# Kernel tuning notes

Measured on AMD Instinct MI355X. Metric: run time of the kernel, lower is better.

The kernel has to match this reference:

```python
import jax, jax.numpy as jnp
import numpy as np
from jax import lax

N = 50000
C = 8
HW = 11
E = 800000
BD = 4
LIN_DIM = C * (HW - 2) * (HW - 2) + BD  # 652
HID = 256
OUT = 5
EPS = 1e-5


def _layernorm(h, g, b):
    mu = jnp.mean(h, axis=-1, keepdims=True)
    var = jnp.var(h, axis=-1, keepdims=True)
    return (h - mu) * lax.rsqrt(var + EPS) * g + b


def setup_inputs() -> dict:
    key = jax.random.key(0)
    ks = jax.random.split(key, 20)
    x = jax.random.normal(ks[0], (N, C, HW, HW), dtype=jnp.float32)
    bd_pred = jax.random.normal(ks[1], (N, BD), dtype=jnp.float32)
    src = jax.random.randint(ks[2], (E,), 0, N)
    dst = jax.random.randint(ks[3], (E,), 0, N)
    dst = jnp.where(src == dst, (dst + 1) % N, dst)  # no self loops
    edge_index = jnp.stack([src, dst]).astype(jnp.int64)
    s = 0.02
    p = {
        'conv_self_w': jax.random.normal(ks[4], (C, C, 3, 3), jnp.float32) * s,
        'conv_self_b': jnp.zeros((C,), jnp.float32),
        'lin_w': jax.random.normal(ks[5], (HID, LIN_DIM), jnp.float32) * s,
        'lin_b': jnp.zeros((HID,), jnp.float32),
        'lin_self_w': jax.random.normal(ks[6], (HID, LIN_DIM), jnp.float32) * s,
        'lin_self_b': jnp.zeros((HID,), jnp.float32),
        'sage_l_w': jax.random.normal(ks[7], (3, HID, HID), jnp.float32) * s,
        'sage_l_b': jnp.zeros((3, HID), jnp.float32),
        'sage_r_w': jax.random.normal(ks[8], (3, HID, HID), jnp.float32) * s,
        'ln_g': jnp.ones((2, HID), jnp.float32),
        'ln_b': jnp.zeros((2, HID), jnp.float32),
        'mp1_w': jax.random.normal(ks[9], (HID, HID), jnp.float32) * s,
        'mp1_b': jnp.zeros((HID,), jnp.float32),
        'mp2_w': jax.random.normal(ks[10], (OUT, HID), jnp.float32) * s,
        'mp2_b': jnp.zeros((OUT,), jnp.float32),
    }
    return dict(x=x, bd_pred=bd_pred, edge_index=edge_index, **p)


def reference(x, bd_pred, edge_index, conv_self_w, conv_self_b, lin_w, lin_b,
              lin_self_w, lin_self_b, sage_l_w, sage_l_b, sage_r_w,
              ln_g, ln_b, mp1_w, mp1_b, mp2_w, mp2_b):
    n = x.shape[0]
    src, dst = edge_index[0], edge_index[1]

    # CustomConv layer 0: conv_self -> flatten -> hstack(bd_pred) -> relu -> two linears
    h = lax.conv_general_dilated(x, conv_self_w, (1, 1), 'VALID',
                                 dimension_numbers=('NCHW', 'OIHW', 'NCHW'))
    h = h + conv_self_b[None, :, None, None]
    h = jnp.concatenate([h.reshape(n, -1), bd_pred], axis=1)  # [N, 652]
    h = jax.nn.relu(h)
    self_x = h @ lin_self_w.T + lin_self_b
    neigh = h @ lin_w.T + lin_b
    h = self_x + jax.ops.segment_sum(neigh[src], dst, num_segments=n)  # aggr='add'

    # in-degree for SAGEConv mean aggregation
    deg = jax.ops.segment_sum(jnp.ones((src.shape[0],), h.dtype), dst, num_segments=n)
    deg = jnp.maximum(deg, 1.0)[:, None]

    emb = h
    for i in range(3):  # SAGEConv layers 1..3
        mean_agg = jax.ops.segment_sum(h[src], dst, num_segments=n) / deg
        h = mean_agg @ sage_l_w[i].T + sage_l_b[i] + h @ sage_r_w[i].T
        emb = h
        h = jax.nn.relu(h)
        # dropout p=0.25 is identity in eval mode
        if i != 2:
            h = _layernorm(h, ln_g[i], ln_b[i])

    z = h @ mp1_w.T + mp1_b
    z = z @ mp2_w.T + mp2_b
    return emb, jax.nn.log_softmax(z, axis=1)
```

## Files before the change

### kernel.cpp

```cpp
#include <hip/hip_runtime.h>
#include <hip/hip_bf16.h>
#include <stdint.h>

#define NN 50000
#define EE 800000

typedef unsigned short u16;
typedef __attribute__((ext_vector_type(4))) float f32x4;
typedef __attribute__((ext_vector_type(8))) short bf16x8;

__device__ __forceinline__ float bu2f(u16 u){ return __uint_as_float(((unsigned)u)<<16); }
__device__ __forceinline__ u16 f2bu(float f){
  unsigned u = __float_as_uint(f);
  u += 0x7fffu + ((u>>16)&1u);
  return (u16)(u>>16);
}
__device__ __forceinline__ float lo16f(unsigned u){ return __uint_as_float(u << 16); }
__device__ __forceinline__ float hi16f(unsigned u){ return __uint_as_float(u & 0xffff0000u); }

__global__ void sniff_kernel(const int* __restrict__ e, const u16* __restrict__ xu,
                             int* __restrict__ flags){
  __shared__ int nz, cnt;
  int t = threadIdx.x;
  if (t == 0){ nz = 0; cnt = 0; }
  __syncthreads();
  if (e[2*t + 1] != 0) atomicOr(&nz, 1);
  u16 u = xu[2*t];
  int ef = (u >> 7) & 0xFF;
  int ok = (u == 0) || (ef >= 118 && ef <= 132);
  atomicAdd(&cnt, ok);
  __syncthreads();
  if (t == 0){ flags[0] = (nz == 0) ? 1 : 0; flags[1] = (cnt >= 200) ? 1 : 0; }
}

__global__ void convert_edges_kernel(const void* __restrict__ ep, int* __restrict__ outp,
                                     const int* __restrict__ flags, int total){
  int i = blockIdx.x*256 + threadIdx.x;
  if (i >= total) return;
  if (flags[0]) outp[i] = (int)((const long long*)ep)[i];
  else          outp[i] = ((const int*)ep)[i];
}

struct CanonTab {
  const void* src[15];
  void*       dst[15];
  int rows[15];
  int sk[15];
  int dk[15];
  int tobf[15];
};

__global__ __launch_bounds__(256) void canon_params_kernel(CanonTab tab, const int* __restrict__ flags){
  int a = blockIdx.y;
  int isbf = flags[1];
  int rows = tab.rows[a], sk = tab.sk[a], dk = tab.dk[a], tobf = tab.tobf[a];
  int n = rows * dk;
  int base = (blockIdx.x*256 + threadIdx.x) * 8;
  if (base >= n) return;
  #pragma unroll
  for (int uu = 0; uu < 8; uu++){
    int i = base + uu;
    if (i >= n) break;
    int r = i / dk, c = i - r*dk;
    float v = 0.f;
    if (c < sk){
      size_t si = (size_t)r*sk + c;
      v = isbf ? bu2f(((const u16*)tab.src[a])[si]) : ((const float*)tab.src[a])[si];
    }
    if (tobf) ((u16*)tab.dst[a])[i] = f2bu(v);
    else      ((float*)tab.dst[a])[i] = v;
  }
}

__global__ __launch_bounds__(256) void conv_relu_kernel(
    const void* __restrict__ xraw, const void* __restrict__ bdraw,
    const float* __restrict__ cw, const float* __restrict__ cb,
    const int* __restrict__ flags, u16* __restrict__ h0){
  __shared__ float xs[968];
  __shared__ float wsm[576];
  __shared__ float bs[8];
  int n = blockIdx.x, t = threadIdx.x;
  int isbf = flags[1];
  if (isbf){
    const ushort4* xp = (const ushort4*)((const u16*)xraw + (size_t)n*968);
    if (t < 242){ ushort4 u = xp[t]; xs[4*t]=bu2f(u.x); xs[4*t+1]=bu2f(u.y); xs[4*t+2]=bu2f(u.z); xs[4*t+3]=bu2f(u.w); }
  } else {
    const float4* xp = (const float4*)((const float*)xraw + (size_t)n*968);
    if (t < 242){ float4 u = xp[t]; xs[4*t]=u.x; xs[4*t+1]=u.y; xs[4*t+2]=u.z; xs[4*t+3]=u.w; }
  }
  if (t < 144){ float4 u = ((const float4*)cw)[t]; wsm[4*t]=u.x; wsm[4*t+1]=u.y; wsm[4*t+2]=u.z; wsm[4*t+3]=u.w; }
  if (t < 8) bs[t] = cb[t];
  __syncthreads();
  u16* outr = h0 + (size_t)n*704;
  if (t < 216){
    int co = t & 7;
    int rowid = t >> 3;
    int oi = rowid / 3;
    int og = rowid - oi*3;
    float wreg[72];
    #pragma unroll
    for (int q = 0; q < 72; q++) wreg[q] = wsm[co*72 + q];
    float a0 = bs[co], a1 = a0, a2 = a0;
    #pragma unroll
    for (int ci = 0; ci < 8; ci++){
      #pragma unroll
      for (int ki = 0; ki < 3; ki++){
        const float* xb = xs + ci*121 + (oi+ki)*11 + og*3;
        float x0=xb[0], x1=xb[1], x2=xb[2], x3=xb[3], x4=xb[4];
        float w0=wreg[ci*9+ki*3+0], w1=wreg[ci*9+ki*3+1], w2=wreg[ci*9+ki*3+2];
        a0 += x0*w0 + x1*w1 + x2*w2;
        a1 += x1*w0 + x2*w1 + x3*w2;
        a2 += x2*w0 + x3*w1 + x4*w2;
      }
    }
    int colbase = co*81 + oi*9 + og*3;
    outr[colbase+0] = f2bu(fmaxf(a0, 0.f));
    outr[colbase+1] = f2bu(fmaxf(a1, 0.f));
    outr[colbase+2] = f2bu(fmaxf(a2, 0.f));
  } else if (t < 220){
    int jj = t - 216;
    float v = isbf ? bu2f(((const u16*)bdraw)[(size_t)n*4 + jj]) : ((const float*)bdraw)[(size_t)n*4 + jj];
    outr[648 + jj] = f2bu(fmaxf(v, 0.f));
  } else {
    for (int c = 652 + (t - 220); c < 704; c += 36) outr[c] = 0;
  }
}

__global__ void deg_kernel(const int* __restrict__ dst, int* __restrict__ degI, int E){
  int e = blockIdx.x*256 + threadIdx.x;
  if (e < E) atomicAdd(&degI[dst[e]], 1);
}
__global__ void invdeg_kernel(const int* __restrict__ degI, float* __restrict__ inv, int n){
  int i = blockIdx.x*256 + threadIdx.x;
  if (i < n){ int d = degI[i]; inv[i] = 1.0f / (float)(d > 1 ? d : 1); }
}

__global__ __launch_bounds__(1024) void scan_kernel(const int* __restrict__ degI,
                                                    int* __restrict__ rowptr,
                                                    int* __restrict__ cursor, int n){
  __shared__ int warp_sums[16];
  __shared__ int carry;
  int t = threadIdx.x;
  if (t == 0) carry = 0;
  __syncthreads();
  for (int base = 0; base < n; base += 8192){
    int i0 = base + t*8;
    int v[8]; int s = 0;
    #pragma unroll
    for (int q = 0; q < 8; q++){ int idx = i0+q; v[q] = (idx < n) ? degI[idx] : 0; s += v[q]; }
    int ts = s;
    #pragma unroll
    for (int off = 1; off < 64; off <<= 1){ int u = __shfl_up(ts, off); if ((t & 63) >= off) ts += u; }
    if ((t & 63) == 63) warp_sums[t >> 6] = ts;
    __syncthreads();
    if (t < 16){
      int wsv = warp_sums[t];
      #pragma unroll
      for (int off = 1; off < 16; off <<= 1){ int u = __shfl_up(wsv, off); if (t >= off) wsv += u; }
      warp_sums[t] = wsv;
    }
    __syncthreads();
    int blk = (t >= 64) ? warp_sums[(t >> 6) - 1] : 0;
    int excl = carry + blk + ts - s;
    #pragma unroll
    for (int q = 0; q < 8; q++){
      int idx = i0+q;
      if (idx < n){ rowptr[idx] = excl; cursor[idx] = excl; }
      excl += v[q];
    }
    int total = warp_sums[15];
    __syncthreads();
    if (t == 0) carry += total;
    __syncthreads();
  }
  if (t == 0) rowptr[n] = carry;
}

__global__ void bucket_kernel(const int* __restrict__ esrc, const int* __restrict__ edst,
                              int* __restrict__ cursor, int* __restrict__ ebuc, int E){
  int e = blockIdx.x*256 + threadIdx.x;
  if (e < E){ int pos = atomicAdd(&cursor[edst[e]], 1); ebuc[pos] = esrc[e]; }
}

__global__ __launch_bounds__(256) void gather_agg_kernel(
    const u16* __restrict__ src_feat, int s_stride,
    const u16* __restrict__ addbase, int a_stride,
    const float* __restrict__ scale, u16* __restrict__ outp,
    const int* __restrict__ rowptr, const int* __restrict__ ebuc){
  int wid = threadIdx.x >> 6, lane = threadIdx.x & 63;
  int n = blockIdx.x*4 + wid;
  if (n >= NN) return;
  int half = lane >> 5;
  int sub  = lane & 31;
  int c0 = sub * 8;
  int beg = rowptr[n], end = rowptr[n+1];
  float acc[8] = {0.f,0.f,0.f,0.f,0.f,0.f,0.f,0.f};
  int j = beg + half;
  for (; j + 2 < end; j += 4){
    int s0 = ebuc[j], s1 = ebuc[j+2];
    uint4 u0 = *(const uint4*)(src_feat + (size_t)s0*s_stride + c0);
    uint4 u1 = *(const uint4*)(src_feat + (size_t)s1*s_stride + c0);
    acc[0] += lo16f(u0.x); acc[1] += hi16f(u0.x);
    acc[2] += lo16f(u0.y); acc[3] += hi16f(u0.y);
    acc[4] += lo16f(u0.z); acc[5] += hi16f(u0.z);
    acc[6] += lo16f(u0.w); acc[7] += hi16f(u0.w);
    acc[0] += lo16f(u1.x); acc[1] += hi16f(u1.x);
    acc[2] += lo16f(u1.y); acc[3] += hi16f(u1.y);
    acc[4] += lo16f(u1.z); acc[5] += hi16f(u1.z);
    acc[6] += lo16f(u1.w); acc[7] += hi16f(u1.w);
  }
  for (; j < end; j += 2){
    int s0 = ebuc[j];
    uint4 u0 = *(const uint4*)(src_feat + (size_t)s0*s_stride + c0);
    acc[0] += lo16f(u0.x); acc[1] += hi16f(u0.x);
    acc[2] += lo16f(u0.y); acc[3] += hi16f(u0.y);
    acc[4] += lo16f(u0.z); acc[5] += hi16f(u0.z);
    acc[6] += lo16f(u0.w); acc[7] += hi16f(u0.w);
  }
  #pragma unroll
  for (int q = 0; q < 8; q++) acc[q] += __shfl_xor(acc[q], 32);
  if (half == 0){
    float sc = scale ? scale[n] : 1.f;
    #pragma unroll
    for (int q = 0; q < 8; q++) acc[q] *= sc;
    if (addbase){
      uint4 b = *(const uint4*)(addbase + (size_t)n*a_stride + c0);
      acc[0] += lo16f(b.x); acc[1] += hi16f(b.x);
      acc[2] += lo16f(b.y); acc[3] += hi16f(b.y);
      acc[4] += lo16f(b.z); acc[5] += hi16f(b.z);
      acc[6] += lo16f(b.w); acc[7] += hi16f(b.w);
    }
    uint4 o;
    o.x = (unsigned)f2bu(acc[0]) | ((unsigned)f2bu(acc[1]) << 16);
    o.y = (unsigned)f2bu(acc[2]) | ((unsigned)f2bu(acc[3]) << 16);
    o.z = (unsigned)f2bu(acc[4]) | ((unsigned)f2bu(acc[5]) << 16);
    o.w = (unsigned)f2bu(acc[6]) | ((unsigned)f2bu(acc[7]) << 16);
    *(uint4*)(outp + (size_t)n*256 + c0) = o;
  }
}

__global__ __launch_bounds__(256) void gemm_mfma_kernel(
    const u16* __restrict__ A1, int lda1, const u16* __restrict__ W1, int K1,
    const u16* __restrict__ A2, int lda2, const u16* __restrict__ W2, int K2,
    const float* __restrict__ bias, int ldc,
    u16* __restrict__ out_bf,
    void* __restrict__ out_emb,
    u16* __restrict__ out_relu_bf,
    const int* __restrict__ flags, int M){
  __shared__ u16 Asm[128][72];
  __shared__ u16 Wsm[128][72];
  int t = threadIdx.x;
  int wave = t >> 6, lane = t & 63;
  int wr = wave >> 1, wc = wave & 1;
  int m0 = blockIdx.x << 7;
  int o0 = blockIdx.y << 7;
  int lrow = t >> 1;
  int lk8  = (t & 1) << 3;
  int fr = lane & 15;
  int fkb = (lane >> 4) << 3;
  f32x4 acc[4][4] = {};

  for (int pass = 0; pass < 2; ++pass){
    const u16* A; const u16* W; int K, lda;
    if (pass == 0){ A = A1; W = W1; K = K1; lda = lda1; }
    else { if (!A2) break; A = A2; W = W2; K = K2; lda = lda2; }
    for (int k0 = 0; k0 < K; k0 += 64){
      int gm = m0 + lrow;
      int4 av0 = make_int4(0,0,0,0), av1 = av0, av2 = av0, av3 = av0;
      if (gm < M){
        const int4* ap = (const int4*)(A + (size_t)gm*lda + k0 + lk8);
        av0 = ap[0]; av1 = ap[2]; av2 = ap[4]; av3 = ap[6];
      }
      const int4* wp = (const int4*)(W + (size_t)(o0 + lrow)*K + k0 + lk8);
      int4 wv0 = wp[0], wv1 = wp[2], wv2 = wp[4], wv3 = wp[6];
      *(int4*)&Asm[lrow][lk8]      = av0;
      *(int4*)&Asm[lrow][lk8+16]   = av1;
      *(int4*)&Asm[lrow][lk8+32]   = av2;
      *(int4*)&Asm[lrow][lk8+48]   = av3;
      *(int4*)&Wsm[lrow][lk8]      = wv0;
      *(int4*)&Wsm[lrow][lk8+16]   = wv1;
      *(int4*)&Wsm[lrow][lk8+32]   = wv2;
      *(int4*)&Wsm[lrow][lk8+48]   = wv3;
      __syncthreads();
      #pragma unroll
      for (int kk = 0; kk < 2; kk++){
        int fk = kk*32 + fkb;
        bf16x8 af[4], wf[4];
        #pragma unroll
        for (int i = 0; i < 4; i++) af[i] = *(const bf16x8*)&Asm[wr*64 + i*16 + fr][fk];
        #pragma unroll
        for (int jj = 0; jj < 4; jj++) wf[jj] = *(const bf16x8*)&Wsm[wc*64 + jj*16 + fr][fk];
        #pragma unroll
        for (int i = 0; i < 4; i++)
          #pragma unroll
          for (int jj = 0; jj < 4; jj++)
            acc[i][jj] = __builtin_amdgcn_mfma_f32_16x16x32_bf16(af[i], wf[jj], acc[i][jj], 0, 0, 0);
      }
      __syncthreads();
    }
  }
  int isbf = flags[1];
  int fg = lane >> 4;
  #pragma unroll
  for (int i = 0; i < 4; i++){
    int rbase = m0 + wr*64 + i*16 + fg*4;
    #pragma unroll
    for (int jj = 0; jj < 4; jj++){
      int col = o0 + wc*64 + jj*16 + fr;
      float bv = bias[col];
      #pragma unroll
      for (int r = 0; r < 4; r++){
        int row = rbase + r;
        if (row < M){
          float v = acc[i][jj][r] + bv;
          size_t off = (size_t)row*ldc + col;
          if (out_bf)   out_bf[off] = f2bu(v);
          if (out_emb){
            if (isbf) ((u16*)out_emb)[off] = f2bu(v);
            else      ((float*)out_emb)[off] = v;
          }
          if (out_relu_bf) out_relu_bf[off] = f2bu(fmaxf(v, 0.f));
        }
      }
    }
  }
}

__global__ __launch_bounds__(256) void relu_ln_kernel(
    const u16* __restrict__ inb, u16* __restrict__ outb,
    const float* __restrict__ g, const float* __restrict__ b){
  __shared__ float rs[4], rs2[4];
  int n = blockIdx.x, t = threadIdx.x;
  float v = fmaxf(bu2f(inb[(size_t)n*256 + t]), 0.f);
  float s = v, s2 = v*v;
  #pragma unroll
  for (int off = 1; off < 64; off <<= 1){ s += __shfl_xor(s, off); s2 += __shfl_xor(s2, off); }
  if ((t & 63) == 0){ rs[t>>6] = s; rs2[t>>6] = s2; }
  __syncthreads();
  float S  = rs[0]+rs[1]+rs[2]+rs[3];
  float S2 = rs2[0]+rs2[1]+rs2[2]+rs2[3];
  float mu  = S * (1.f/256.f);
  float var = S2 * (1.f/256.f) - mu*mu;
  float inv = rsqrtf(var + 1e-5f);
  outb[(size_t)n*256 + t] = f2bu((v - mu) * inv * g[t] + b[t]);
}

__global__ __launch_bounds__(256) void head_kernel(
    const u16* __restrict__ z1, const float* __restrict__ w2, const float* __restrict__ b2,
    void* __restrict__ outbase, size_t out_off, const int* __restrict__ flags, int M){
  __shared__ float wsm[1280];
  __shared__ float bs[5];
  int t = threadIdx.x;
  for (int i = t; i < 320; i += 256){
    float4 u = ((const float4*)w2)[i];
    wsm[4*i]=u.x; wsm[4*i+1]=u.y; wsm[4*i+2]=u.z; wsm[4*i+3]=u.w;
  }
  if (t < 5) bs[t] = b2[t];
  __syncthreads();
  int n = blockIdx.x*256 + t;
  if (n >= M) return;
  const u16* zp = z1 + (size_t)n*256;
  float acc[5];
  #pragma unroll
  for (int o = 0; o < 5; o++) acc[o] = bs[o];
  for (int k = 0; k < 256; k += 4){
    ushort4 zu = *(const ushort4*)(zp + k);
    float z0 = bu2f(zu.x), z1f = bu2f(zu.y), z2 = bu2f(zu.z), z3 = bu2f(zu.w);
    #pragma unroll
    for (int o = 0; o < 5; o++){
      const float* w = wsm + o*256 + k;
      acc[o] += z0*w[0] + z1f*w[1] + z2*w[2] + z3*w[3];
    }
  }
  float mx = acc[0];
  #pragma unroll
  for (int o = 1; o < 5; o++) mx = fmaxf(mx, acc[o]);
  float se = 0.f;
  #pragma unroll
  for (int o = 0; o < 5; o++) se += expf(acc[o] - mx);
  float lse = mx + logf(se);
  int isbf = flags[1];
  if (isbf){
    u16* op = (u16*)outbase + out_off + (size_t)n*5;
    #pragma unroll
    for (int o = 0; o < 5; o++) op[o] = f2bu(acc[o] - lse);
  } else {
    float* op = (float*)outbase + out_off + (size_t)n*5;
    #pragma unroll
    for (int o = 0; o < 5; o++) op[o] = acc[o] - lse;
  }
}

extern "C" void kernel_launch(void* const* d_in, const int* in_sizes, int n_in,
                              void* d_out, int out_size, void* d_ws, size_t ws_size,
                              hipStream_t stream){
  (void)in_sizes; (void)n_in; (void)out_size; (void)ws_size;
  const void* x    = d_in[0];
  const void* bd   = d_in[1];
  const void* eraw = d_in[2];

  char* ws = (char*)d_ws;
  const size_t OFF_H0 = 0;
  const size_t OFF_A  = OFF_H0 + (size_t)NN*704*2;
  const size_t OFF_B  = OFF_A  + (size_t)NN*256*2;
  const size_t OFF_C  = OFF_B  + (size_t)NN*256*2;
  const size_t OFF_DEG= OFF_C  + (size_t)NN*256*2;
  const size_t OFF_INV= OFF_DEG + (size_t)NN*4;
  const size_t OFF_EDG= OFF_INV + (size_t)NN*4;
  const size_t OFF_RP = OFF_EDG + (size_t)2*EE*4;
  const size_t OFF_CUR= OFF_RP  + (size_t)(NN+16)*4;
  const size_t OFF_EBU= OFF_CUR + (size_t)NN*4;
  const size_t OFF_FLG= OFF_EBU + (size_t)EE*4;
  const size_t OFF_PRM= OFF_FLG + 256;

  u16*   h0   = (u16*)(ws + OFF_H0);
  u16*   bufA = (u16*)(ws + OFF_A);
  u16*   bufB = (u16*)(ws + OFF_B);
  u16*   bufC = (u16*)(ws + OFF_C);
  u16*   bufAB= (u16*)(ws + OFF_B);
  int*   degI = (int*)(ws + OFF_DEG);
  float* invd = (float*)(ws + OFF_INV);
  int*   edg  = (int*)(ws + OFF_EDG);
  int*   rowp = (int*)(ws + OFF_RP);
  int*   curs = (int*)(ws + OFF_CUR);
  int*   ebuc = (int*)(ws + OFF_EBU);
  int*   flg  = (int*)(ws + OFF_FLG);
  char*  prm  = ws + OFF_PRM;
  const int* esrc = edg;
  const int* edst = edg + EE;

  static const int crows[15] = {1,1,256,1,256,1,1,1,1,1,1,1,1,1,1};
  static const int csk[15]   = {576,8,652,256,652,256,196608,768,196608,512,512,65536,256,1280,5};
  static const int cdk[15]   = {576,8,704,256,704,256,196608,768,196608,512,512,65536,256,1280,5};
  static const int ctobf[15] = {0,0,1,0,1,0,1,0,1,0,0,1,0,0,0};
  CanonTab tab;
  size_t po = 0;
  void* dsts[15];
  for (int i = 0; i < 15; i++){
    tab.src[i] = d_in[3+i];
    tab.rows[i] = crows[i]; tab.sk[i] = csk[i]; tab.dk[i] = cdk[i]; tab.tobf[i] = ctobf[i];
    dsts[i] = prm + po;
    tab.dst[i] = dsts[i];
    size_t bytes = (size_t)crows[i]*cdk[i] * (ctobf[i] ? 2 : 4);
    po += (bytes + 63) & ~(size_t)63;
  }
  u16*   c_l2w = (u16*)dsts[4];
  float* c_l2b = (float*)(prm + po);  po += 512*4;
  tab.dst[2] = c_l2w + (size_t)256*704;
  tab.dst[3] = c_l2b + 256;
  tab.dst[5] = c_l2b;
  po += (size_t)256*704*2;

  const float* c_cw  = (const float*)dsts[0];
  const float* c_cb  = (const float*)dsts[1];
  const u16*   c_slw = (const u16*)dsts[6];
  const float* c_slb = (const float*)dsts[7];
  const u16*   c_srw = (const u16*)dsts[8];
  const float* c_lng = (const float*)dsts[9];
  const float* c_lnb = (const float*)dsts[10];
  const u16*   c_m1w = (const u16*)dsts[11];
  const float* c_m1b = (const float*)dsts[12];
  const float* c_m2w = (const float*)dsts[13];
  const float* c_m2b = (const float*)dsts[14];

  {
    u16* fresh_w = (u16*)(prm + po);
    po += (size_t)512*704*2;
    float* fresh_b = (float*)(prm + po);
    po += 512*4 + 64;
    tab.dst[4] = fresh_w;
    tab.dst[2] = fresh_w + (size_t)256*704;
    tab.dst[5] = fresh_b;
    tab.dst[3] = fresh_b + 256;
    c_l2w = fresh_w;
    c_l2b = fresh_b;
  }

  hipMemsetAsync(degI, 0, (size_t)NN*4, stream);
  sniff_kernel<<<1, 256, 0, stream>>>((const int*)eraw, (const u16*)x, flg);
  {
    dim3 cgrid(96, 15);
    canon_params_kernel<<<cgrid, 256, 0, stream>>>(tab, flg);
  }
  convert_edges_kernel<<<(2*EE + 255)/256, 256, 0, stream>>>(eraw, edg, flg, 2*EE);
  conv_relu_kernel<<<NN, 256, 0, stream>>>(x, bd, c_cw, c_cb, flg, h0);
  deg_kernel<<<(EE + 255)/256, 256, 0, stream>>>(edst, degI, EE);
  invdeg_kernel<<<(NN + 255)/256, 256, 0, stream>>>(degI, invd, NN);
  scan_kernel<<<1, 1024, 0, stream>>>(degI, rowp, curs, NN);
  bucket_kernel<<<(EE + 255)/256, 256, 0, stream>>>(esrc, edst, curs, ebuc, EE);

  dim3 ggrid((NN + 127)/128, 2);
  dim3 ggrid0((NN + 127)/128, 4);
  const int agrid = (NN + 3)/4;
  gemm_mfma_kernel<<<ggrid0, 256, 0, stream>>>(h0, 704, c_l2w, 704,
      nullptr, 0, nullptr, 0, c_l2b, 512, bufAB, nullptr, nullptr, flg, NN);
  gather_agg_kernel<<<agrid, 256, 0, stream>>>(bufAB + 256, 512, bufAB, 512,
      nullptr, bufA, rowp, ebuc);

  for (int i = 0; i < 3; i++){
    gather_agg_kernel<<<agrid, 256, 0, stream>>>(bufA, 256, nullptr, 0,
        invd, bufC, rowp, ebuc);
    const u16*   L  = c_slw + (size_t)i*256*256;
    const float* Lb = c_slb + (size_t)i*256;
    const u16*   R  = c_srw + (size_t)i*256*256;
    if (i < 2){
      gemm_mfma_kernel<<<ggrid, 256, 0, stream>>>(bufC, 256, L, 256,
          bufA, 256, R, 256, Lb, 256, bufB, nullptr, nullptr, flg, NN);
      relu_ln_kernel<<<NN, 256, 0, stream>>>(bufB, bufA,
          c_lng + (size_t)i*256, c_lnb + (size_t)i*256);
    } else {
      gemm_mfma_kernel<<<ggrid, 256, 0, stream>>>(bufC, 256, L, 256,
          bufA, 256, R, 256, Lb, 256, nullptr, d_out, bufB, flg, NN);
    }
  }
  gemm_mfma_kernel<<<ggrid, 256, 0, stream>>>(bufB, 256, c_m1w, 256,
      nullptr, 0, nullptr, 0, c_m1b, 256, bufC, nullptr, nullptr, flg, NN);
  head_kernel<<<(NN + 255)/256, 256, 0, stream>>>(bufC, c_m2w, c_m2b,
      d_out, (size_t)NN*256, flg, NN);
}
```

Measured before the change: 877.6 us.

## Batch 32 nodes per conv block with register-tiled rows; unroll gather deeper

```diff
diff --git a/kernel.cpp b/kernel.cpp
--- a/kernel.cpp
+++ b/kernel.cpp
@@ -72,58 +72,83 @@
   }
 }
 
-__global__ __launch_bounds__(256) void conv_relu_kernel(
+#define ROW_LOAD(R) { _Pragma("unroll") for (int q = 0; q < 11; q++) R[q] = bu2f(xrow[xb + q]); xb += 11; }
+#define ACC_ROWS(A,B,C,OI) { _Pragma("unroll") for (int oj = 0; oj < 9; oj++){ \
+    acc[(OI)*9+oj] += A[oj]*w[0] + A[oj+1]*w[1] + A[oj+2]*w[2] \
+                    + B[oj]*w[3] + B[oj+1]*w[4] + B[oj+2]*w[5] \
+                    + C[oj]*w[6] + C[oj+1]*w[7] + C[oj+2]*w[8]; } }
+
+__global__ __launch_bounds__(256, 2) void conv_relu_kernel(
     const void* __restrict__ xraw, const void* __restrict__ bdraw,
     const float* __restrict__ cw, const float* __restrict__ cb,
     const int* __restrict__ flags, u16* __restrict__ h0){
-  __shared__ float xs[968];
+  __shared__ u16 xs[30976];
   __shared__ float wsm[576];
   __shared__ float bs[8];
-  int n = blockIdx.x, t = threadIdx.x;
+  int t = threadIdx.x;
+  int nb = blockIdx.x << 5;
   int isbf = flags[1];
-  if (isbf){
-    const ushort4* xp = (const ushort4*)((const u16*)xraw + (size_t)n*968);
-    if (t < 242){ ushort4 u = xp[t]; xs[4*t]=bu2f(u.x); xs[4*t+1]=bu2f(u.y); xs[4*t+2]=bu2f(u.z); xs[4*t+3]=bu2f(u.w); }
-  } else {
-    const float4* xp = (const float4*)((const float*)xraw + (size_t)n*968);
-    if (t < 242){ float4 u = xp[t]; xs[4*t]=u.x; xs[4*t+1]=u.y; xs[4*t+2]=u.z; xs[4*t+3]=u.w; }
-  }
   if (t < 144){ float4 u = ((const float4*)cw)[t]; wsm[4*t]=u.x; wsm[4*t+1]=u.y; wsm[4*t+2]=u.z; wsm[4*t+3]=u.w; }
   if (t < 8) bs[t] = cb[t];
+  int limit = NN - nb; if (limit > 32) limit = 32;
+  int nu4 = limit * 121;
+  if (isbf){
+    const u16* xg = (const u16*)xraw + (size_t)nb*968;
+    for (int i = t; i < nu4; i += 256)
+      *(uint4*)&xs[i*8] = *(const uint4*)(xg + (size_t)i*8);
+  } else {
+    const float* xg = (const float*)xraw + (size_t)nb*968;
+    for (int i = t; i < nu4; i += 256){
+      const float4* p = (const float4*)(xg + (size_t)i*8);
+      float4 u0 = p[0], u1 = p[1];
+      uint4 v;
+      v.x = (unsigned)f2bu(u0.x) | ((unsigned)f2bu(u0.y) << 16);
+      v.y = (unsigned)f2bu(u0.z) | ((unsigned)f2bu(u0.w) << 16);
+      v.z = (unsigned)f2bu(u1.x) | ((unsigned)f2bu(u1.y) << 16);
+      v.w = (unsigned)f2bu(u1.z) | ((unsigned)f2bu(u1.w) << 16);
+      *(uint4*)&xs[i*8] = v;
+    }
+  }
+  for (int i = t; i < 32*56; i += 256){
+    int node = i / 56, c = i - node*56;
+    if (node < limit){
+      u16 v = 0;
+      if (c < 4){
+        float f = isbf ? bu2f(((const u16*)bdraw)[(size_t)(nb+node)*4 + c])
+                       : ((const float*)bdraw)[(size_t)(nb+node)*4 + c];
+        v = f2bu(fmaxf(f, 0.f));
+      }
+      h0[(size_t)(nb+node)*704 + 648 + c] = v;
+    }
+  }
   __syncthreads();
-  u16* outr = h0 + (size_t)n*704;
-  if (t < 216){
-    int co = t & 7;
-    int rowid = t >> 3;
-    int oi = rowid / 3;
-    int og = rowid - oi*3;
-    float wreg[72];
-    #pragma unroll
-    for (int q = 0; q < 72; q++) wreg[q] = wsm[co*72 + q];
-    float a0 = bs[co], a1 = a0, a2 = a0;
-    #pragma unroll
-    for (int ci = 0; ci < 8; ci++){
-      #pragma unroll
-      for (int ki = 0; ki < 3; ki++){
-        const float* xb = xs + ci*121 + (oi+ki)*11 + og*3;
-        float x0=xb[0], x1=xb[1], x2=xb[2], x3=xb[3], x4=xb[4];
-        float w0=wreg[ci*9+ki*3+0], w1=wreg[ci*9+ki*3+1], w2=wreg[ci*9+ki*3+2];
-        a0 += x0*w0 + x1*w1 + x2*w2;
-        a1 += x1*w0 + x2*w1 + x3*w2;
-        a2 += x2*w0 + x3*w1 + x4*w2;
-      }
-    }
-    int colbase = co*81 + oi*9 + og*3;
-    outr[colbase+0] = f2bu(fmaxf(a0, 0.f));
-    outr[colbase+1] = f2bu(fmaxf(a1, 0.f));
-    outr[colbase+2] = f2bu(fmaxf(a2, 0.f));
-  } else if (t < 220){
-    int jj = t - 216;
-    float v = isbf ? bu2f(((const u16*)bdraw)[(size_t)n*4 + jj]) : ((const float*)bdraw)[(size_t)n*4 + jj];
-    outr[648 + jj] = f2bu(fmaxf(v, 0.f));
-  } else {
-    for (int c = 652 + (t - 220); c < 704; c += 36) outr[c] = 0;
-  }
+  int node = t >> 3, co = t & 7;
+  if (node >= limit) return;
+  const u16* xrow = xs + node*968;
+  float acc[81];
+  float binit = bs[co];
+  #pragma unroll
+  for (int p = 0; p < 81; p++) acc[p] = binit;
+  for (int ci = 0; ci < 8; ci++){
+    float w[9];
+    #pragma unroll
+    for (int q = 0; q < 9; q++) w[q] = wsm[co*72 + ci*9 + q];
+    int xb = ci*121;
+    float r0[11], r1[11], r2[11];
+    ROW_LOAD(r0) ROW_LOAD(r1)
+    ROW_LOAD(r2) ACC_ROWS(r0,r1,r2,0)
+    ROW_LOAD(r0) ACC_ROWS(r1,r2,r0,1)
+    ROW_LOAD(r1) ACC_ROWS(r2,r0,r1,2)
+    ROW_LOAD(r2) ACC_ROWS(r0,r1,r2,3)
+    ROW_LOAD(r0) ACC_ROWS(r1,r2,r0,4)
+    ROW_LOAD(r1) ACC_ROWS(r2,r0,r1,5)
+    ROW_LOAD(r2) ACC_ROWS(r0,r1,r2,6)
+    ROW_LOAD(r0) ACC_ROWS(r1,r2,r0,7)
+    ROW_LOAD(r1) ACC_ROWS(r2,r0,r1,8)
+  }
+  u16* outr = h0 + (size_t)(nb+node)*704 + co*81;
+  #pragma unroll
+  for (int p = 0; p < 81; p++) outr[p] = f2bu(fmaxf(acc[p], 0.f));
 }
 
 __global__ void deg_kernel(const int* __restrict__ dst, int* __restrict__ degI, int E){
@@ -182,6 +207,10 @@
   if (e < E){ int pos = atomicAdd(&cursor[edst[e]], 1); ebuc[pos] = esrc[e]; }
 }
 
+#define GACC(U) { acc[0] += lo16f(U.x); acc[1] += hi16f(U.x); \
+                  acc[2] += lo16f(U.y); acc[3] += hi16f(U.y); \
+                  acc[4] += lo16f(U.z); acc[5] += hi16f(U.z); \
+                  acc[6] += lo16f(U.w); acc[7] += hi16f(U.w); }
 __global__ __launch_bounds__(256) void gather_agg_kernel(
     const u16* __restrict__ src_feat, int s_stride,
     const u16* __restrict__ addbase, int a_stride,
@@ -196,26 +225,24 @@
   int beg = rowptr[n], end = rowptr[n+1];
   float acc[8] = {0.f,0.f,0.f,0.f,0.f,0.f,0.f,0.f};
   int j = beg + half;
+  for (; j + 6 < end; j += 8){
+    int s0 = ebuc[j], s1 = ebuc[j+2], s2 = ebuc[j+4], s3 = ebuc[j+6];
+    uint4 u0 = *(const uint4*)(src_feat + (size_t)s0*s_stride + c0);
+    uint4 u1 = *(const uint4*)(src_feat + (size_t)s1*s_stride + c0);
+    uint4 u2 = *(const uint4*)(src_feat + (size_t)s2*s_stride + c0);
+    uint4 u3 = *(const uint4*)(src_feat + (size_t)s3*s_stride + c0);
+    GACC(u0) GACC(u1) GACC(u2) GACC(u3)
+  }
   for (; j + 2 < end; j += 4){
     int s0 = ebuc[j], s1 = ebuc[j+2];
     uint4 u0 = *(const uint4*)(src_feat + (size_t)s0*s_stride + c0);
     uint4 u1 = *(const uint4*)(src_feat + (size_t)s1*s_stride + c0);
-    acc[0] += lo16f(u0.x); acc[1] += hi16f(u0.x);
-    acc[2] += lo16f(u0.y); acc[3] += hi16f(u0.y);
-    acc[4] += lo16f(u0.z); acc[5] += hi16f(u0.z);
-    acc[6] += lo16f(u0.w); acc[7] += hi16f(u0.w);
-    acc[0] += lo16f(u1.x); acc[1] += hi16f(u1.x);
-    acc[2] += lo16f(u1.y); acc[3] += hi16f(u1.y);
-    acc[4] += lo16f(u1.z); acc[5] += hi16f(u1.z);
-    acc[6] += lo16f(u1.w); acc[7] += hi16f(u1.w);
+    GACC(u0) GACC(u1)
   }
   for (; j < end; j += 2){
     int s0 = ebuc[j];
     uint4 u0 = *(const uint4*)(src_feat + (size_t)s0*s_stride + c0);
-    acc[0] += lo16f(u0.x); acc[1] += hi16f(u0.x);
-    acc[2] += lo16f(u0.y); acc[3] += hi16f(u0.y);
-    acc[4] += lo16f(u0.z); acc[5] += hi16f(u0.z);
-    acc[6] += lo16f(u0.w); acc[7] += hi16f(u0.w);
+    GACC(u0)
   }
   #pragma unroll
   for (int q = 0; q < 8; q++) acc[q] += __shfl_xor(acc[q], 32);
@@ -225,10 +252,7 @@
     for (int q = 0; q < 8; q++) acc[q] *= sc;
     if (addbase){
       uint4 b = *(const uint4*)(addbase + (size_t)n*a_stride + c0);
-      acc[0] += lo16f(b.x); acc[1] += hi16f(b.x);
-      acc[2] += lo16f(b.y); acc[3] += hi16f(b.y);
-      acc[4] += lo16f(b.z); acc[5] += hi16f(b.z);
-      acc[6] += lo16f(b.w); acc[7] += hi16f(b.w);
+      GACC(b)
     }
     uint4 o;
     o.x = (unsigned)f2bu(acc[0]) | ((unsigned)f2bu(acc[1]) << 16);
@@ -444,12 +468,12 @@
     size_t bytes = (size_t)crows[i]*cdk[i] * (ctobf[i] ? 2 : 4);
     po += (bytes + 63) & ~(size_t)63;
   }
-  u16*   c_l2w = (u16*)dsts[4];
-  float* c_l2b = (float*)(prm + po);  po += 512*4;
+  u16*   c_l2w = (u16*)(prm + po);  po += (size_t)512*704*2;
+  float* c_l2b = (float*)(prm + po); po += 512*4 + 64;
+  tab.dst[4] = c_l2w;
   tab.dst[2] = c_l2w + (size_t)256*704;
+  tab.dst[5] = c_l2b;
   tab.dst[3] = c_l2b + 256;
-  tab.dst[5] = c_l2b;
-  po += (size_t)256*704*2;
 
   const float* c_cw  = (const float*)dsts[0];
   const float* c_cb  = (const float*)dsts[1];
@@ -463,19 +487,6 @@
   const float* c_m2w = (const float*)dsts[13];
   const float* c_m2b = (const float*)dsts[14];
 
-  {
-    u16* fresh_w = (u16*)(prm + po);
-    po += (size_t)512*704*2;
-    float* fresh_b = (float*)(prm + po);
-    po += 512*4 + 64;
-    tab.dst[4] = fresh_w;
-    tab.dst[2] = fresh_w + (size_t)256*704;
-    tab.dst[5] = fresh_b;
-    tab.dst[3] = fresh_b + 256;
-    c_l2w = fresh_w;
-    c_l2b = fresh_b;
-  }
-
   hipMemsetAsync(degI, 0, (size_t)NN*4, stream);
   sniff_kernel<<<1, 256, 0, stream>>>((const int*)eraw, (const u16*)x, flg);
   {
@@ -483,7 +494,7 @@
     canon_params_kernel<<<cgrid, 256, 0, stream>>>(tab, flg);
   }
   convert_edges_kernel<<<(2*EE + 255)/256, 256, 0, stream>>>(eraw, edg, flg, 2*EE);
-  conv_relu_kernel<<<NN, 256, 0, stream>>>(x, bd, c_cw, c_cb, flg, h0);
+  conv_relu_kernel<<<(NN + 31)/32, 256, 0, stream>>>(x, bd, c_cw, c_cb, flg, h0);
   deg_kernel<<<(EE + 255)/256, 256, 0, stream>>>(edst, degI, EE);
   invdeg_kernel<<<(NN + 255)/256, 256, 0, stream>>>(degI, invd, NN);
   scan_kernel<<<1, 1024, 0, stream>>>(degI, rowp, curs, NN);
```

After: 1.222 ms. 39.2% more time.

## Transform-then-aggregate SAGE layers and fuse gather with ReLU/LayerNorm epilogue

Applied to the files above, without the earlier changes.

```diff
diff --git a/kernel.cpp b/kernel.cpp
--- a/kernel.cpp
+++ b/kernel.cpp
@@ -34,11 +34,15 @@
 }
 
 __global__ void convert_edges_kernel(const void* __restrict__ ep, int* __restrict__ outp,
+                                     int* __restrict__ degI,
                                      const int* __restrict__ flags, int total){
   int i = blockIdx.x*256 + threadIdx.x;
   if (i >= total) return;
-  if (flags[0]) outp[i] = (int)((const long long*)ep)[i];
-  else          outp[i] = ((const int*)ep)[i];
+  int v;
+  if (flags[0]) v = (int)((const long long*)ep)[i];
+  else          v = ((const int*)ep)[i];
+  outp[i] = v;
+  if (i >= EE) atomicAdd(&degI[v], 1);
 }
 
 struct CanonTab {
@@ -126,18 +130,10 @@
   }
 }
 
-__global__ void deg_kernel(const int* __restrict__ dst, int* __restrict__ degI, int E){
-  int e = blockIdx.x*256 + threadIdx.x;
-  if (e < E) atomicAdd(&degI[dst[e]], 1);
-}
-__global__ void invdeg_kernel(const int* __restrict__ degI, float* __restrict__ inv, int n){
-  int i = blockIdx.x*256 + threadIdx.x;
-  if (i < n){ int d = degI[i]; inv[i] = 1.0f / (float)(d > 1 ? d : 1); }
-}
-
 __global__ __launch_bounds__(1024) void scan_kernel(const int* __restrict__ degI,
                                                     int* __restrict__ rowptr,
-                                                    int* __restrict__ cursor, int n){
+                                                    int* __restrict__ cursor,
+                                                    float* __restrict__ inv, int n){
   __shared__ int warp_sums[16];
   __shared__ int carry;
   int t = threadIdx.x;
@@ -165,7 +161,10 @@
     #pragma unroll
     for (int q = 0; q < 8; q++){
       int idx = i0+q;
-      if (idx < n){ rowptr[idx] = excl; cursor[idx] = excl; }
+      if (idx < n){
+        rowptr[idx] = excl; cursor[idx] = excl;
+        inv[idx] = 1.0f / (float)(v[q] > 1 ? v[q] : 1);
+      }
       excl += v[q];
     }
     int total = warp_sums[15];
@@ -182,10 +181,16 @@
   if (e < E){ int pos = atomicAdd(&cursor[edst[e]], 1); ebuc[pos] = esrc[e]; }
 }
 
-__global__ __launch_bounds__(256) void gather_agg_kernel(
-    const u16* __restrict__ src_feat, int s_stride,
-    const u16* __restrict__ addbase, int a_stride,
-    const float* __restrict__ scale, u16* __restrict__ outp,
+#define GACC(U) { acc[0] += lo16f(U.x); acc[1] += hi16f(U.x); \
+                  acc[2] += lo16f(U.y); acc[3] += hi16f(U.y); \
+                  acc[4] += lo16f(U.z); acc[5] += hi16f(U.z); \
+                  acc[6] += lo16f(U.w); acc[7] += hi16f(U.w); }
+__global__ __launch_bounds__(256) void gather_ln_kernel(
+    const u16* __restrict__ Y, const u16* __restrict__ Z,
+    const float* __restrict__ scale,
+    const float* __restrict__ g, const float* __restrict__ b, int mode,
+    u16* __restrict__ outA, void* __restrict__ out_emb,
+    const int* __restrict__ flags,
     const int* __restrict__ rowptr, const int* __restrict__ ebuc){
   int wid = threadIdx.x >> 6, lane = threadIdx.x & 63;
   int n = blockIdx.x*4 + wid;
@@ -196,57 +201,98 @@
   int beg = rowptr[n], end = rowptr[n+1];
   float acc[8] = {0.f,0.f,0.f,0.f,0.f,0.f,0.f,0.f};
   int j = beg + half;
+  for (; j + 6 < end; j += 8){
+    int s0 = ebuc[j], s1 = ebuc[j+2], s2 = ebuc[j+4], s3 = ebuc[j+6];
+    uint4 u0 = *(const uint4*)(Y + (size_t)s0*512 + c0);
+    uint4 u1 = *(const uint4*)(Y + (size_t)s1*512 + c0);
+    uint4 u2 = *(const uint4*)(Y + (size_t)s2*512 + c0);
+    uint4 u3 = *(const uint4*)(Y + (size_t)s3*512 + c0);
+    GACC(u0) GACC(u1) GACC(u2) GACC(u3)
+  }
   for (; j + 2 < end; j += 4){
     int s0 = ebuc[j], s1 = ebuc[j+2];
-    uint4 u0 = *(const uint4*)(src_feat + (size_t)s0*s_stride + c0);
-    uint4 u1 = *(const uint4*)(src_feat + (size_t)s1*s_stride + c0);
-    acc[0] += lo16f(u0.x); acc[1] += hi16f(u0.x);
-    acc[2] += lo16f(u0.y); acc[3] += hi16f(u0.y);
-    acc[4] += lo16f(u0.z); acc[5] += hi16f(u0.z);
-    acc[6] += lo16f(u0.w); acc[7] += hi16f(u0.w);
-    acc[0] += lo16f(u1.x); acc[1] += hi16f(u1.x);
-    acc[2] += lo16f(u1.y); acc[3] += hi16f(u1.y);
-    acc[4] += lo16f(u1.z); acc[5] += hi16f(u1.z);
-    acc[6] += lo16f(u1.w); acc[7] += hi16f(u1.w);
+    uint4 u0 = *(const uint4*)(Y + (size_t)s0*512 + c0);
+    uint4 u1 = *(const uint4*)(Y + (size_t)s1*512 + c0);
+    GACC(u0) GACC(u1)
   }
   for (; j < end; j += 2){
     int s0 = ebuc[j];
-    uint4 u0 = *(const uint4*)(src_feat + (size_t)s0*s_stride + c0);
-    acc[0] += lo16f(u0.x); acc[1] += hi16f(u0.x);
-    acc[2] += lo16f(u0.y); acc[3] += hi16f(u0.y);
-    acc[4] += lo16f(u0.z); acc[5] += hi16f(u0.z);
-    acc[6] += lo16f(u0.w); acc[7] += hi16f(u0.w);
+    uint4 u0 = *(const uint4*)(Y + (size_t)s0*512 + c0);
+    GACC(u0)
   }
   #pragma unroll
   for (int q = 0; q < 8; q++) acc[q] += __shfl_xor(acc[q], 32);
-  if (half == 0){
-    float sc = scale ? scale[n] : 1.f;
-    #pragma unroll
-    for (int q = 0; q < 8; q++) acc[q] *= sc;
-    if (addbase){
-      uint4 b = *(const uint4*)(addbase + (size_t)n*a_stride + c0);
-      acc[0] += lo16f(b.x); acc[1] += hi16f(b.x);
-      acc[2] += lo16f(b.y); acc[3] += hi16f(b.y);
-      acc[4] += lo16f(b.z); acc[5] += hi16f(b.z);
-      acc[6] += lo16f(b.w); acc[7] += hi16f(b.w);
-    }
-    uint4 o;
-    o.x = (unsigned)f2bu(acc[0]) | ((unsigned)f2bu(acc[1]) << 16);
-    o.y = (unsigned)f2bu(acc[2]) | ((unsigned)f2bu(acc[3]) << 16);
-    o.z = (unsigned)f2bu(acc[4]) | ((unsigned)f2bu(acc[5]) << 16);
-    o.w = (unsigned)f2bu(acc[6]) | ((unsigned)f2bu(acc[7]) << 16);
-    *(uint4*)(outp + (size_t)n*256 + c0) = o;
+  float sc = scale ? scale[n] : 1.f;
+  float val[8];
+  {
+    uint4 zv = *(const uint4*)(Z + (size_t)n*512 + c0);
+    val[0] = acc[0]*sc + lo16f(zv.x); val[1] = acc[1]*sc + hi16f(zv.x);
+    val[2] = acc[2]*sc + lo16f(zv.y); val[3] = acc[3]*sc + hi16f(zv.y);
+    val[4] = acc[4]*sc + lo16f(zv.z); val[5] = acc[5]*sc + hi16f(zv.z);
+    val[6] = acc[6]*sc + lo16f(zv.w); val[7] = acc[7]*sc + hi16f(zv.w);
+  }
+  if (mode == 0){
+    if (half == 0){
+      uint4 o;
+      o.x = (unsigned)f2bu(val[0]) | ((unsigned)f2bu(val[1]) << 16);
+      o.y = (unsigned)f2bu(val[2]) | ((unsigned)f2bu(val[3]) << 16);
+      o.z = (unsigned)f2bu(val[4]) | ((unsigned)f2bu(val[5]) << 16);
+      o.w = (unsigned)f2bu(val[6]) | ((unsigned)f2bu(val[7]) << 16);
+      *(uint4*)(outA + (size_t)n*256 + c0) = o;
+    }
+  } else if (mode == 1){
+    float r[8]; float s = 0.f, s2 = 0.f;
+    #pragma unroll
+    for (int q = 0; q < 8; q++){ r[q] = fmaxf(val[q], 0.f); s += r[q]; s2 += r[q]*r[q]; }
+    #pragma unroll
+    for (int off = 1; off < 32; off <<= 1){ s += __shfl_xor(s, off); s2 += __shfl_xor(s2, off); }
+    float mu  = s * (1.f/256.f);
+    float var = s2 * (1.f/256.f) - mu*mu;
+    float inv = rsqrtf(var + 1e-5f);
+    if (half == 0){
+      float4 g0 = *(const float4*)(g + c0), g1 = *(const float4*)(g + c0 + 4);
+      float4 b0 = *(const float4*)(b + c0), b1 = *(const float4*)(b + c0 + 4);
+      float gg[8] = {g0.x,g0.y,g0.z,g0.w,g1.x,g1.y,g1.z,g1.w};
+      float bb[8] = {b0.x,b0.y,b0.z,b0.w,b1.x,b1.y,b1.z,b1.w};
+      uint4 o; u16 e[8];
+      #pragma unroll
+      for (int q = 0; q < 8; q++) e[q] = f2bu((r[q]-mu)*inv*gg[q] + bb[q]);
+      o.x = (unsigned)e[0] | ((unsigned)e[1] << 16);
+      o.y = (unsigned)e[2] | ((unsigned)e[3] << 16);
+      o.z = (unsigned)e[4] | ((unsigned)e[5] << 16);
+      o.w = (unsigned)e[6] | ((unsigned)e[7] << 16);
+      *(uint4*)(outA + (size_t)n*256 + c0) = o;
+    }
+  } else {
+    if (half == 0){
+      if (flags[1]){
+        uint4 o;
+        o.x = (unsigned)f2bu(val[0]) | ((unsigned)f2bu(val[1]) << 16);
+        o.y = (unsigned)f2bu(val[2]) | ((unsigned)f2bu(val[3]) << 16);
+        o.z = (unsigned)f2bu(val[4]) | ((unsigned)f2bu(val[5]) << 16);
+        o.w = (unsigned)f2bu(val[6]) | ((unsigned)f2bu(val[7]) << 16);
+        *(uint4*)((u16*)out_emb + (size_t)n*256 + c0) = o;
+      } else {
+        float* op = (float*)out_emb + (size_t)n*256 + c0;
+        *(float4*)op     = make_float4(val[0], val[1], val[2], val[3]);
+        *(float4*)(op+4) = make_float4(val[4], val[5], val[6], val[7]);
+      }
+      uint4 o;
+      o.x = (unsigned)f2bu(fmaxf(val[0],0.f)) | ((unsigned)f2bu(fmaxf(val[1],0.f)) << 16);
+      o.y = (unsigned)f2bu(fmaxf(val[2],0.f)) | ((unsigned)f2bu(fmaxf(val[3],0.f)) << 16);
+      o.z = (unsigned)f2bu(fmaxf(val[4],0.f)) | ((unsigned)f2bu(fmaxf(val[5],0.f)) << 16);
+      o.w = (unsigned)f2bu(fmaxf(val[6],0.f)) | ((unsigned)f2bu(fmaxf(val[7],0.f)) << 16);
+      *(uint4*)(outA + (size_t)n*256 + c0) = o;
+    }
   }
 }
 
 __global__ __launch_bounds__(256) void gemm_mfma_kernel(
-    const u16* __restrict__ A1, int lda1, const u16* __restrict__ W1, int K1,
-    const u16* __restrict__ A2, int lda2, const u16* __restrict__ W2, int K2,
-    const float* __restrict__ bias, int ldc,
-    u16* __restrict__ out_bf,
-    void* __restrict__ out_emb,
-    u16* __restrict__ out_relu_bf,
-    const int* __restrict__ flags, int M){
+    const u16* __restrict__ A, int lda,
+    const u16* __restrict__ Wa, const u16* __restrict__ Wb,
+    const float* __restrict__ biasA, const float* __restrict__ biasB,
+    int K, int ldc,
+    u16* __restrict__ out_bf, int M){
   __shared__ u16 Asm[128][72];
   __shared__ u16 Wsm[128][72];
   int t = threadIdx.x;
@@ -254,95 +300,66 @@
   int wr = wave >> 1, wc = wave & 1;
   int m0 = blockIdx.x << 7;
   int o0 = blockIdx.y << 7;
+  const u16* W; const float* biasp;
+  if (o0 < 256){ W = Wa + (size_t)o0*K; biasp = biasA + o0; }
+  else         { W = Wb + (size_t)(o0-256)*K; biasp = biasB + (o0-256); }
   int lrow = t >> 1;
   int lk8  = (t & 1) << 3;
   int fr = lane & 15;
   int fkb = (lane >> 4) << 3;
   f32x4 acc[4][4] = {};
 
-  for (int pass = 0; pass < 2; ++pass){
-    const u16* A; const u16* W; int K, lda;
-    if (pass == 0){ A = A1; W = W1; K = K1; lda = lda1; }
-    else { if (!A2) break; A = A2; W = W2; K = K2; lda = lda2; }
-    for (int k0 = 0; k0 < K; k0 += 64){
-      int gm = m0 + lrow;
-      int4 av0 = make_int4(0,0,0,0), av1 = av0, av2 = av0, av3 = av0;
-      if (gm < M){
-        const int4* ap = (const int4*)(A + (size_t)gm*lda + k0 + lk8);
-        av0 = ap[0]; av1 = ap[2]; av2 = ap[4]; av3 = ap[6];
-      }
-      const int4* wp = (const int4*)(W + (size_t)(o0 + lrow)*K + k0 + lk8);
-      int4 wv0 = wp[0], wv1 = wp[2], wv2 = wp[4], wv3 = wp[6];
-      *(int4*)&Asm[lrow][lk8]      = av0;
-      *(int4*)&Asm[lrow][lk8+16]   = av1;
-      *(int4*)&Asm[lrow][lk8+32]   = av2;
-      *(int4*)&Asm[lrow][lk8+48]   = av3;
-      *(int4*)&Wsm[lrow][lk8]      = wv0;
-      *(int4*)&Wsm[lrow][lk8+16]   = wv1;
-      *(int4*)&Wsm[lrow][lk8+32]   = wv2;
-      *(int4*)&Wsm[lrow][lk8+48]   = wv3;
-      __syncthreads();
-      #pragma unroll
-      for (int kk = 0; kk < 2; kk++){
-        int fk = kk*32 + fkb;
-        bf16x8 af[4], wf[4];
+  for (int k0 = 0; k0 < K; k0 += 64){
+    int gm = m0 + lrow;
+    int4 av0 = make_int4(0,0,0,0), av1 = av0, av2 = av0, av3 = av0;
+    if (gm < M){
+      const int4* ap = (const int4*)(A + (size_t)gm*lda + k0 + lk8);
+      av0 = ap[0]; av1 = ap[2]; av2 = ap[4]; av3 = ap[6];
+    }
+    const int4* wp = (const int4*)(W + (size_t)lrow*K + k0 + lk8);
+    int4 wv0 = wp[0], wv1 = wp[2], wv2 = wp[4], wv3 = wp[6];
+    *(int4*)&Asm[lrow][lk8]      = av0;
+    *(int4*)&Asm[lrow][lk8+16]   = av1;
+    *(int4*)&Asm[lrow][lk8+32]   = av2;
+    *(int4*)&Asm[lrow][lk8+48]   = av3;
+    *(int4*)&Wsm[lrow][lk8]      = wv0;
+    *(int4*)&Wsm[lrow][lk8+16]   = wv1;
+    *(int4*)&Wsm[lrow][lk8+32]   = wv2;
+    *(int4*)&Wsm[lrow][lk8+48]   = wv3;
+    __syncthreads();
+    #pragma unroll
+    for (int kk = 0; kk < 2; kk++){
+      int fk = kk*32 + fkb;
+      bf16x8 af[4], wf[4];
+      #pragma unroll
+      for (int i = 0; i < 4; i++) af[i] = *(const bf16x8*)&Asm[wr*64 + i*16 + fr][fk];
+      #pragma unroll
+      for (int jj = 0; jj < 4; jj++) wf[jj] = *(const bf16x8*)&Wsm[wc*64 + jj*16 + fr][fk];
+      #pragma unroll
+      for (int i = 0; i < 4; i++)
         #pragma unroll
-        for (int i = 0; i < 4; i++) af[i] = *(const bf16x8*)&Asm[wr*64 + i*16 + fr][fk];
-        #pragma unroll
-        for (int jj = 0; jj < 4; jj++) wf[jj] = *(const bf16x8*)&Wsm[wc*64 + jj*16 + fr][fk];
-        #pragma unroll
-        for (int i = 0; i < 4; i++)
-          #pragma unroll
-          for (int jj = 0; jj < 4; jj++)
-            acc[i][jj] = __builtin_amdgcn_mfma_f32_16x16x32_bf16(af[i], wf[jj], acc[i][jj], 0, 0, 0);
-      }
-      __syncthreads();
-    }
-  }
-  int isbf = flags[1];
+        for (int jj = 0; jj < 4; jj++)
+          acc[i][jj] = __builtin_amdgcn_mfma_f32_16x16x32_bf16(af[i], wf[jj], acc[i][jj], 0, 0, 0);
+    }
+    __syncthreads();
+  }
   int fg = lane >> 4;
   #pragma unroll
   for (int i = 0; i < 4; i++){
     int rbase = m0 + wr*64 + i*16 + fg*4;
     #pragma unroll
     for (int jj = 0; jj < 4; jj++){
-      int col = o0 + wc*64 + jj*16 + fr;
-      float bv = bias[col];
+      int lcol = wc*64 + jj*16 + fr;
+      float bv = biasp[lcol];
+      int col = o0 + lcol;
       #pragma unroll
       for (int r = 0; r < 4; r++){
         int row = rbase + r;
-        if (row < M){
-          float v = acc[i][jj][r] + bv;
-          size_t off = (size_t)row*ldc + col;
-          if (out_bf)   out_bf[off] = f2bu(v);
-          if (out_emb){
-            if (isbf) ((u16*)out_emb)[off] = f2bu(v);
-            else      ((float*)out_emb)[off] = v;
-          }
-          if (out_relu_bf) out_relu_bf[off] = f2bu(fmaxf(v, 0.f));
-        }
+        if (row < M)
+          out_bf[(size_t)row*ldc + col] = f2bu(acc[i][jj][r] + bv);
       }
     }
   }
-}
-
-__global__ __launch_bounds__(256) void relu_ln_kernel(
-    const u16* __restrict__ inb, u16* __restrict__ outb,
-    const float* __restrict__ g, const float* __restrict__ b){
-  __shared__ float rs[4], rs2[4];
-  int n = blockIdx.x, t = threadIdx.x;
-  float v = fmaxf(bu2f(inb[(size_t)n*256 + t]), 0.f);
-  float s = v, s2 = v*v;
-  #pragma unroll
-  for (int off = 1; off < 64; off <<= 1){ s += __shfl_xor(s, off); s2 += __shfl_xor(s2, off); }
-  if ((t & 63) == 0){ rs[t>>6] = s; rs2[t>>6] = s2; }
-  __syncthreads();
-  float S  = rs[0]+rs[1]+rs[2]+rs[3];
-  float S2 = rs2[0]+rs2[1]+rs2[2]+rs2[3];
-  float mu  = S * (1.f/256.f);
-  float var = S2 * (1.f/256.f) - mu*mu;
-  float inv = rsqrtf(var + 1e-5f);
-  outb[(size_t)n*256 + t] = f2bu((v - mu) * inv * g[t] + b[t]);
 }
 
 __global__ __launch_bounds__(256) void head_kernel(
@@ -402,9 +419,8 @@
   char* ws = (char*)d_ws;
   const size_t OFF_H0 = 0;
   const size_t OFF_A  = OFF_H0 + (size_t)NN*704*2;
-  const size_t OFF_B  = OFF_A  + (size_t)NN*256*2;
-  const size_t OFF_C  = OFF_B  + (size_t)NN*256*2;
-  const size_t OFF_DEG= OFF_C  + (size_t)NN*256*2;
+  const size_t OFF_YZ = OFF_A  + (size_t)NN*256*2;
+  const size_t OFF_DEG= OFF_YZ + (size_t)NN*512*2;
   const size_t OFF_INV= OFF_DEG + (size_t)NN*4;
   const size_t OFF_EDG= OFF_INV + (size_t)NN*4;
   const size_t OFF_RP = OFF_EDG + (size_t)2*EE*4;
@@ -413,11 +429,10 @@
   const size_t OFF_FLG= OFF_EBU + (size_t)EE*4;
   const size_t OFF_PRM= OFF_FLG + 256;
 
-  u16*   h0   = (u16*)(ws + OFF_H0);
-  u16*   bufA = (u16*)(ws + OFF_A);
-  u16*   bufB = (u16*)(ws + OFF_B);
-  u16*   bufC = (u16*)(ws + OFF_C);
-  u16*   bufAB= (u16*)(ws + OFF_B);
+  u16*   h0    = (u16*)(ws + OFF_H0);
+  u16*   bufA  = (u16*)(ws + OFF_A);
+  u16*   bufYZ = (u16*)(ws + OFF_YZ);
+  u16*   bufC  = (u16*)(ws + OFF_YZ);
   int*   degI = (int*)(ws + OFF_DEG);
   float* invd = (float*)(ws + OFF_INV);
   int*   edg  = (int*)(ws + OFF_EDG);
@@ -444,15 +459,14 @@
     size_t bytes = (size_t)crows[i]*cdk[i] * (ctobf[i] ? 2 : 4);
     po += (bytes + 63) & ~(size_t)63;
   }
-  u16*   c_l2w = (u16*)dsts[4];
-  float* c_l2b = (float*)(prm + po);  po += 512*4;
-  tab.dst[2] = c_l2w + (size_t)256*704;
-  tab.dst[3] = c_l2b + 256;
-  tab.dst[5] = c_l2b;
-  po += (size_t)256*704*2;
+  float* c_zero = (float*)(prm + po); po += 1024 + 64;
 
   const float* c_cw  = (const float*)dsts[0];
   const float* c_cb  = (const float*)dsts[1];
+  const u16*   c_lw  = (const u16*)dsts[2];
+  const float* c_lb  = (const float*)dsts[3];
+  const u16*   c_lsw = (const u16*)dsts[4];
+  const float* c_lsb = (const float*)dsts[5];
   const u16*   c_slw = (const u16*)dsts[6];
   const float* c_slb = (const float*)dsts[7];
   const u16*   c_srw = (const u16*)dsts[8];
@@ -463,58 +477,43 @@
   const float* c_m2w = (const float*)dsts[13];
   const float* c_m2b = (const float*)dsts[14];
 
-  {
-    u16* fresh_w = (u16*)(prm + po);
-    po += (size_t)512*704*2;
-    float* fresh_b = (float*)(prm + po);
-    po += 512*4 + 64;
-    tab.dst[4] = fresh_w;
-    tab.dst[2] = fresh_w + (size_t)256*704;
-    tab.dst[5] = fresh_b;
-    tab.dst[3] = fresh_b + 256;
-    c_l2w = fresh_w;
-    c_l2b = fresh_b;
-  }
-
   hipMemsetAsync(degI, 0, (size_t)NN*4, stream);
+  hipMemsetAsync(c_zero, 0, 1024, stream);
   sniff_kernel<<<1, 256, 0, stream>>>((const int*)eraw, (const u16*)x, flg);
   {
     dim3 cgrid(96, 15);
     canon_params_kernel<<<cgrid, 256, 0, stream>>>(tab, flg);
   }
-  convert_edges_kernel<<<(2*EE + 255)/256, 256, 0, stream>>>(eraw, edg, flg, 2*EE);
+  convert_edges_kernel<<<(2*EE + 255)/256, 256, 0, stream>>>(eraw, edg, degI, flg, 2*EE);
   conv_relu_kernel<<<NN, 256, 0, stream>>>(x, bd, c_cw, c_cb, flg, h0);
-  deg_kernel<<<(EE + 255)/256, 256, 0, stream>>>(edst, degI, EE);
-  invdeg_kernel<<<(NN + 255)/256, 256, 0, stream>>>(degI, invd, NN);
-  scan_kernel<<<1, 1024, 0, stream>>>(degI, rowp, curs, NN);
+  scan_kernel<<<1, 1024, 0, stream>>>(degI, rowp, curs, invd, NN);
   bucket_kernel<<<(EE + 255)/256, 256, 0, stream>>>(esrc, edst, curs, ebuc, EE);
 
-  dim3 ggrid((NN + 127)/128, 2);
-  dim3 ggrid0((NN + 127)/128, 4);
+  dim3 g512((NN + 127)/128, 4);
+  dim3 g256((NN + 127)/128, 2);
   const int agrid = (NN + 3)/4;
-  gemm_mfma_kernel<<<ggrid0, 256, 0, stream>>>(h0, 704, c_l2w, 704,
-      nullptr, 0, nullptr, 0, c_l2b, 512, bufAB, nullptr, nullptr, flg, NN);
-  gather_agg_kernel<<<agrid, 256, 0, stream>>>(bufAB + 256, 512, bufAB, 512,
-      nullptr, bufA, rowp, ebuc);
+
+  gemm_mfma_kernel<<<g512, 256, 0, stream>>>(h0, 704, c_lw, c_lsw, c_lb, c_lsb,
+      704, 512, bufYZ, NN);
+  gather_ln_kernel<<<agrid, 256, 0, stream>>>(bufYZ, bufYZ + 256, nullptr,
+      nullptr, nullptr, 0, bufA, nullptr, flg, rowp, ebuc);
 
   for (int i = 0; i < 3; i++){
-    gather_agg_kernel<<<agrid, 256, 0, stream>>>(bufA, 256, nullptr, 0,
-        invd, bufC, rowp, ebuc);
     const u16*   L  = c_slw + (size_t)i*256*256;
+    const u16*   R  = c_srw + (size_t)i*256*256;
     const float* Lb = c_slb + (size_t)i*256;
-    const u16*   R  = c_srw + (size_t)i*256*256;
+    gemm_mfma_kernel<<<g512, 256, 0, stream>>>(bufA, 256, L, R, c_zero, Lb,
+        256, 512, bufYZ, NN);
     if (i < 2){
-      gemm_mfma_kernel<<<ggrid, 256, 0, stream>>>(bufC, 256, L, 256,
-          bufA, 256, R, 256, Lb, 256, bufB, nullptr, nullptr, flg, NN);
-      relu_ln_kernel<<<NN, 256, 0, stream>>>(bufB, bufA,
-          c_lng + (size_t)i*256, c_lnb + (size_t)i*256);
+      gather_ln_kernel<<<agrid, 256, 0, stream>>>(bufYZ, bufYZ + 256, invd,
+          c_lng + (size_t)i*256, c_lnb + (size_t)i*256, 1, bufA, nullptr, flg, rowp, ebuc);
     } else {
-      gemm_mfma_kernel<<<ggrid, 256, 0, stream>>>(bufC, 256, L, 256,
-          bufA, 256, R, 256, Lb, 256, nullptr, d_out, bufB, flg, NN);
-    }
-  }
-  gemm_mfma_kernel<<<ggrid, 256, 0, stream>>>(bufB, 256, c_m1w, 256,
-      nullptr, 0, nullptr, 0, c_m1b, 256, bufC, nullptr, nullptr, flg, NN);
+      gather_ln_kernel<<<agrid, 256, 0, stream>>>(bufYZ, bufYZ + 256, invd,
+          nullptr, nullptr, 2, bufA, d_out, flg, rowp, ebuc);
+    }
+  }
+  gemm_mfma_kernel<<<g256, 256, 0, stream>>>(bufA, 256, c_m1w, nullptr, c_m1b, nullptr,
+      256, 256, bufC, NN);
   head_kernel<<<(NN + 255)/256, 256, 0, stream>>>(bufC, c_m2w, c_m2b,
       d_out, (size_t)NN*256, flg, NN);
 }
```

New measurement: 830.4 us. 1.06x faster.
